# Optimization experiments

Hardware: AMD Instinct MI355X
Metric: run time of the kernel (lower is better)

## Reference

```python
import jax, jax.numpy as jnp
import numpy as np

B, TE, TD, D, U = 8, 256, 256, 256, 256


def setup_inputs() -> dict:
    key = jax.random.key(0)
    k1, k2, k3, k4, k5 = jax.random.split(key, 5)
    glorot = lambda k, shape: jax.random.uniform(
        k, shape, jnp.float32,
        -np.sqrt(6.0 / (shape[0] + shape[1])), np.sqrt(6.0 / (shape[0] + shape[1])))
    return {
        "en_seq": jax.random.normal(k1, (B, TE, D), jnp.float32),
        "de_seq": jax.random.normal(k2, (B, TD, D), jnp.float32),
        "w_en": glorot(k3, (D, U)),
        "w_de": glorot(k4, (D, U)),
        "nu": glorot(k5, (U, 1)),
    }


def reference(en_seq, de_seq, w_en, w_de, nu):
    # Additive co-attention scores.
    ae = jnp.einsum('bte,eu->btu', en_seq, w_en)          # (B, Te, U)
    ad = jnp.einsum('bsd,du->bsu', de_seq, w_de)          # (B, Td, U)
    # co_m[b, td, te, u] = ae[b, te, u] + ad[b, td, u]  (matches K.repeat / repeat_elements layout)
    co = jnp.tanh(ad[:, :, None, :] + ae[:, None, :, :])  # (B, Td, Te, U)
    mu = jnp.einsum('bstu,ul->bst', co, nu)               # (B, Td, Te)
    alphas = jax.nn.softmax(mu, axis=-1)                  # softmax over en time
    max_mu = jnp.max(mu, axis=-1)                         # (B, Td)
    max_alphas = jax.nn.softmax(max_mu, axis=-1)          # softmax over de time
    h_hat = jnp.sum(de_seq * max_alphas[..., None], axis=1)  # (B, Dd)
    sum_en = jnp.einsum('bst,bte->bse', alphas, en_seq)      # (B, Td, De)
    output = jnp.concatenate(
        [de_seq, sum_en, de_seq * sum_en, de_seq * h_hat[:, None, :]], axis=-1)
    return output  # (B, Td, 4*D)
```

## Files before the change

### kernel.cpp

```cpp
#include <hip/hip_runtime.h>

#define B_   8
#define TE_  256
#define TD_  256
#define D_   256
#define U_   256

#define EET_OFF   0
#define ED_OFF    524288
#define ALPHA_OFF 1048576
#define MAXMU_OFF 1572864
#define HH_OFF    1574912

__device__ __forceinline__ float fexp2(float x) {
#if __has_builtin(__builtin_amdgcn_exp2f)
  return __builtin_amdgcn_exp2f(x);
#else
  return exp2f(x);
#endif
}
__device__ __forceinline__ float frcp(float x) {
#if __has_builtin(__builtin_amdgcn_rcpf)
  return __builtin_amdgcn_rcpf(x);
#else
  return 1.0f / x;
#endif
}

#define LOG2E_F 1.4426950408889634f
#define TWO_LOG2E_F 2.8853900817779268f

__global__ __launch_bounds__(256) void coatt_k1_proj(
    const float* __restrict__ en, const float* __restrict__ de,
    const float* __restrict__ w_en, const float* __restrict__ w_de,
    float* __restrict__ ws) {
  const int which = blockIdx.z;
  const float* __restrict__ A = which ? de : en;
  const float* __restrict__ W = which ? w_de : w_en;
  const int rowBase = blockIdx.y * 64;
  const int colBase = blockIdx.x * 64;
  __shared__ float As[2][32][68];
  __shared__ float Bs[2][32][68];
  const int tid = threadIdx.x;
  const int tx = tid & 15, ty = tid >> 4;

  const int aRow0 = tid >> 3, aC4 = tid & 7;
  const int bK0 = tid >> 4, bC4 = tid & 15;
  float4 aR[2], bR[2];

#pragma unroll
  for (int kk = 0; kk < 2; ++kk) {
    aR[kk] = *(const float4*)&A[(rowBase + aRow0 + 32 * kk) * D_ + aC4 * 4];
    bR[kk] = *(const float4*)&W[(bK0 + 16 * kk) * U_ + colBase + bC4 * 4];
  }
#pragma unroll
  for (int kk = 0; kk < 2; ++kk) {
    float v[4]; *(float4*)v = aR[kk];
#pragma unroll
    for (int j = 0; j < 4; ++j) As[0][aC4 * 4 + j][aRow0 + 32 * kk] = v[j];
    *(float4*)&Bs[0][bK0 + 16 * kk][bC4 * 4] = bR[kk];
  }
  __syncthreads();

  float acc[4][4] = {};
#define K1_COMPUTE(BUF)                                            \
  _Pragma("unroll")                                                \
  for (int k = 0; k < 32; ++k) {                                   \
    float av[4], bv[4];                                            \
    *(float4*)av = *(const float4*)&As[BUF][k][ty * 4];            \
    *(float4*)bv = *(const float4*)&Bs[BUF][k][tx * 4];            \
    _Pragma("unroll")                                              \
    for (int i = 0; i < 4; ++i)                                    \
      _Pragma("unroll")                                            \
      for (int j = 0; j < 4; ++j)                                  \
        acc[i][j] = fmaf(av[i], bv[j], acc[i][j]);                 \
  }

  for (int kc = 0; kc < 7; ++kc) {
    const int k0 = (kc + 1) * 32;
#pragma unroll
    for (int kk = 0; kk < 2; ++kk) {
      aR[kk] = *(const float4*)&A[(rowBase + aRow0 + 32 * kk) * D_ + k0 + aC4 * 4];
      bR[kk] = *(const float4*)&W[(k0 + bK0 + 16 * kk) * U_ + colBase + bC4 * 4];
    }
    const int cur = kc & 1, nxt = cur ^ 1;
    K1_COMPUTE(cur)
#pragma unroll
    for (int kk = 0; kk < 2; ++kk) {
      float v[4]; *(float4*)v = aR[kk];
#pragma unroll
      for (int j = 0; j < 4; ++j) As[nxt][aC4 * 4 + j][aRow0 + 32 * kk] = v[j];
      *(float4*)&Bs[nxt][bK0 + 16 * kk][bC4 * 4] = bR[kk];
    }
    __syncthreads();
  }
  K1_COMPUTE(1)
  __syncthreads();

  if (which) {
    float* __restrict__ out = ws + ED_OFF;
#pragma unroll
    for (int i = 0; i < 4; ++i) {
      float4 o;
      o.x = fexp2(acc[i][0] * TWO_LOG2E_F);
      o.y = fexp2(acc[i][1] * TWO_LOG2E_F);
      o.z = fexp2(acc[i][2] * TWO_LOG2E_F);
      o.w = fexp2(acc[i][3] * TWO_LOG2E_F);
      *(float4*)&out[(rowBase + ty * 4 + i) * U_ + colBase + tx * 4] = o;
    }
  } else {
    float* Cs = &As[0][0][0];
#pragma unroll
    for (int i = 0; i < 4; ++i)
#pragma unroll
      for (int j = 0; j < 4; ++j)
        Cs[(tx * 4 + j) * 68 + ty * 4 + i] = fexp2(acc[i][j] * TWO_LOG2E_F);
    __syncthreads();
    float* __restrict__ out = ws + EET_OFF;
    const int b = rowBase >> 8, t0 = rowBase & 255;
#pragma unroll
    for (int kk = 0; kk < 4; ++kk) {
      const int q = tid + 256 * kk;
      const int uc = q >> 4, tq = q & 15;
      const float4 v = *(const float4*)&Cs[uc * 68 + tq * 4];
      *(float4*)&out[(size_t)(b * U_ + colBase + uc) * TE_ + t0 + tq * 4] = v;
    }
  }
}

__global__ __launch_bounds__(256) void coatt_k2_mu(
    const float* __restrict__ nu, float* __restrict__ ws) {
  const float* __restrict__ EeT = ws + EET_OFF;
  const float* __restrict__ Ed = ws + ED_OFF;
  float* __restrict__ alphas = ws + ALPHA_OFF;
  float* __restrict__ maxmu = ws + MAXMU_OFF;
  const int b = blockIdx.y;
  const int sBase = blockIdx.x * 4;
  const int tid = threadIdx.x;
  const int w = tid >> 6, lane = tid & 63;
  const float* __restrict__ Ee_b = EeT + (size_t)b * U_ * TE_ + tid;
  const float* __restrict__ Ed_b = Ed + (size_t)(b * TD_ + sBase) * U_;

  float acc0 = 0.f, acc1 = 0.f, acc2 = 0.f, acc3 = 0.f;
#pragma unroll 4
  for (int u4 = 0; u4 < 64; ++u4) {
    const float4 nv = *(const float4*)&nu[u4 * 4];
    const float4 e0 = *(const float4*)&Ed_b[0 * U_ + u4 * 4];
    const float4 e1 = *(const float4*)&Ed_b[1 * U_ + u4 * 4];
    const float4 e2 = *(const float4*)&Ed_b[2 * U_ + u4 * 4];
    const float4 e3 = *(const float4*)&Ed_b[3 * U_ + u4 * 4];
    float ee[4];
#pragma unroll
    for (int j = 0; j < 4; ++j) ee[j] = Ee_b[(u4 * 4 + j) * TE_];
    const float* nvp = (const float*)&nv;
    const float* p0 = (const float*)&e0;
    const float* p1 = (const float*)&e1;
    const float* p2 = (const float*)&e2;
    const float* p3 = (const float*)&e3;
#pragma unroll
    for (int j = 0; j < 4; ++j) {
      acc0 = fmaf(nvp[j], frcp(fmaf(p0[j], ee[j], 1.0f)), acc0);
      acc1 = fmaf(nvp[j], frcp(fmaf(p1[j], ee[j], 1.0f)), acc1);
      acc2 = fmaf(nvp[j], frcp(fmaf(p2[j], ee[j], 1.0f)), acc2);
      acc3 = fmaf(nvp[j], frcp(fmaf(p3[j], ee[j], 1.0f)), acc3);
    }
  }
  float v[4] = {-2.f * acc0, -2.f * acc1, -2.f * acc2, -2.f * acc3};
  __shared__ float part[4][4];
  float m[4];
#pragma unroll
  for (int s = 0; s < 4; ++s) {
    m[s] = v[s];
#pragma unroll
    for (int off = 32; off > 0; off >>= 1) m[s] = fmaxf(m[s], __shfl_xor(m[s], off));
    if (lane == 0) part[s][w] = m[s];
  }
  __syncthreads();
#pragma unroll
  for (int s = 0; s < 4; ++s)
    m[s] = fmaxf(fmaxf(part[s][0], part[s][1]), fmaxf(part[s][2], part[s][3]));
  __syncthreads();
  float e[4], sm[4];
#pragma unroll
  for (int s = 0; s < 4; ++s) {
    e[s] = fexp2((v[s] - m[s]) * LOG2E_F);
    sm[s] = e[s];
#pragma unroll
    for (int off = 32; off > 0; off >>= 1) sm[s] += __shfl_xor(sm[s], off);
    if (lane == 0) part[s][w] = sm[s];
  }
  __syncthreads();
  float* __restrict__ al = alphas + (size_t)(b * TD_ + sBase) * TE_;
#pragma unroll
  for (int s = 0; s < 4; ++s) {
    const float tot = (part[s][0] + part[s][1]) + (part[s][2] + part[s][3]);
    al[s * TE_ + tid] = e[s] * frcp(tot);
  }
  if (tid == 0) {
#pragma unroll
    for (int s = 0; s < 4; ++s) maxmu[b * TD_ + sBase + s] = m[s];
  }
}

__global__ __launch_bounds__(256) void coatt_k3_hhat(
    const float* __restrict__ de, float* __restrict__ ws) {
  const float* __restrict__ maxmu = ws + MAXMU_OFF;
  float* __restrict__ hhat = ws + HH_OFF;
  const int b = blockIdx.y;
  const int dBase = blockIdx.x * 32;
  const int tid = threadIdx.x;
  const int w = tid >> 6, lane = tid & 63;
  __shared__ float red[8];
  __shared__ float malpha[256];
  __shared__ float acc_red[256];
  const float v = maxmu[b * TD_ + tid];
  float m = v;
#pragma unroll
  for (int off = 32; off > 0; off >>= 1) m = fmaxf(m, __shfl_xor(m, off));
  if (lane == 0) red[w] = m;
  __syncthreads();
  m = fmaxf(fmaxf(red[0], red[1]), fmaxf(red[2], red[3]));
  const float e = fexp2((v - m) * LOG2E_F);
  float sm = e;
#pragma unroll
  for (int off = 32; off > 0; off >>= 1) sm += __shfl_xor(sm, off);
  if (lane == 0) red[4 + w] = sm;
  __syncthreads();
  sm = (red[4] + red[5]) + (red[6] + red[7]);
  malpha[tid] = e * frcp(sm);
  __syncthreads();
  const int dl = tid & 31, sg = tid >> 5;
  float acc = 0.f;
  for (int s = sg * 32; s < sg * 32 + 32; ++s)
    acc = fmaf(de[(b * TD_ + s) * D_ + dBase + dl], malpha[s], acc);
  acc_red[tid] = acc;
  __syncthreads();
  if (tid < 32) {
    float t = acc_red[tid];
#pragma unroll
    for (int g = 1; g < 8; ++g) t += acc_red[g * 32 + tid];
    hhat[b * D_ + dBase + tid] = t;
  }
}

__global__ __launch_bounds__(256) void coatt_k4_out(
    const float* __restrict__ en, const float* __restrict__ de,
    const float* __restrict__ ws, float* __restrict__ out) {
  const float* __restrict__ alphas = ws + ALPHA_OFF;
  const float* __restrict__ hhat = ws + HH_OFF;
  const int b = blockIdx.y;
  const int sBase = blockIdx.x * 4;
  const int d = threadIdx.x;
  const float* __restrict__ al = alphas + (size_t)(b * TD_ + sBase) * TE_;
  const float* __restrict__ en_b = en + (size_t)b * TE_ * D_ + d;

  float acc0 = 0.f, acc1 = 0.f, acc2 = 0.f, acc3 = 0.f;
#pragma unroll 4
  for (int t4 = 0; t4 < 64; ++t4) {
    const float4 a0 = *(const float4*)&al[0 * TE_ + t4 * 4];
    const float4 a1 = *(const float4*)&al[1 * TE_ + t4 * 4];
    const float4 a2 = *(const float4*)&al[2 * TE_ + t4 * 4];
    const float4 a3 = *(const float4*)&al[3 * TE_ + t4 * 4];
    float env[4];
#pragma unroll
    for (int j = 0; j < 4; ++j) env[j] = en_b[(t4 * 4 + j) * D_];
    const float* q0 = (const float*)&a0;
    const float* q1 = (const float*)&a1;
    const float* q2 = (const float*)&a2;
    const float* q3 = (const float*)&a3;
#pragma unroll
    for (int j = 0; j < 4; ++j) {
      acc0 = fmaf(q0[j], env[j], acc0);
      acc1 = fmaf(q1[j], env[j], acc1);
      acc2 = fmaf(q2[j], env[j], acc2);
      acc3 = fmaf(q3[j], env[j], acc3);
    }
  }
  const float hh = hhat[b * D_ + d];
  const float se[4] = {acc0, acc1, acc2, acc3};
#pragma unroll
  for (int s = 0; s < 4; ++s) {
    const float dd = de[(size_t)(b * TD_ + sBase + s) * D_ + d];
    float* o = out + (size_t)(b * TD_ + sBase + s) * (4 * D_);
    o[d] = dd;
    o[D_ + d] = se[s];
    o[2 * D_ + d] = dd * se[s];
    o[3 * D_ + d] = dd * hh;
  }
}

extern "C" void kernel_launch(void* const* d_in, const int* in_sizes, int n_in,
                              void* d_out, int out_size, void* d_ws, size_t ws_size,
                              hipStream_t stream) {
  (void)in_sizes; (void)n_in; (void)out_size; (void)ws_size;
  const float* en   = (const float*)d_in[0];
  const float* de   = (const float*)d_in[1];
  const float* w_en = (const float*)d_in[2];
  const float* w_de = (const float*)d_in[3];
  const float* nu   = (const float*)d_in[4];
  float* out = (float*)d_out;
  float* ws  = (float*)d_ws;

  coatt_k1_proj<<<dim3(4, 32, 2), 256, 0, stream>>>(en, de, w_en, w_de, ws);
  coatt_k2_mu<<<dim3(64, 8), 256, 0, stream>>>(nu, ws);
  coatt_k3_hhat<<<dim3(8, 8), 256, 0, stream>>>(de, ws);
  coatt_k4_out<<<dim3(64, 8), 256, 0, stream>>>(en, de, ws, out);
}
```

Before: 121.2 us.

## Fuse softmax-weighted sum into mu kernel and vectorize EeT layout

Merges the alpha softmax and the alpha-weighted sum over encoder features into one kernel, so alphas stay in shared memory instead of being written to and re-read from the workspace. The hhat kernel now writes the last output quarter directly, which removes one launch. The projection kernel moves to 512 threads with smaller per-thread tiles, and EeT is stored interleaved in groups of four u so the mu kernel can issue float4 loads. The trade-off is a longer fused kernel with more shared memory and lower per-thread GEMM reuse in the projection.

```diff
diff --git a/kernel.cpp b/kernel.cpp
--- a/kernel.cpp
+++ b/kernel.cpp
@@ -8,9 +8,7 @@
 
 #define EET_OFF   0
 #define ED_OFF    524288
-#define ALPHA_OFF 1048576
-#define MAXMU_OFF 1572864
-#define HH_OFF    1574912
+#define MAXMU_OFF 1048576
 
 __device__ __forceinline__ float fexp2(float x) {
 #if __has_builtin(__builtin_amdgcn_exp2f)
@@ -30,7 +28,7 @@
 #define LOG2E_F 1.4426950408889634f
 #define TWO_LOG2E_F 2.8853900817779268f
 
-__global__ __launch_bounds__(256) void coatt_k1_proj(
+__global__ __launch_bounds__(512) void coatt_k1_proj(
     const float* __restrict__ en, const float* __restrict__ de,
     const float* __restrict__ w_en, const float* __restrict__ w_de,
     float* __restrict__ ws) {
@@ -39,106 +37,99 @@
   const float* __restrict__ W = which ? w_de : w_en;
   const int rowBase = blockIdx.y * 64;
   const int colBase = blockIdx.x * 64;
-  __shared__ float As[2][32][68];
-  __shared__ float Bs[2][32][68];
+  __shared__ float smem[2][2][32][68];
   const int tid = threadIdx.x;
-  const int tx = tid & 15, ty = tid >> 4;
-
-  const int aRow0 = tid >> 3, aC4 = tid & 7;
-  const int bK0 = tid >> 4, bC4 = tid & 15;
-  float4 aR[2], bR[2];
-
-#pragma unroll
-  for (int kk = 0; kk < 2; ++kk) {
-    aR[kk] = *(const float4*)&A[(rowBase + aRow0 + 32 * kk) * D_ + aC4 * 4];
-    bR[kk] = *(const float4*)&W[(bK0 + 16 * kk) * U_ + colBase + bC4 * 4];
-  }
-#pragma unroll
-  for (int kk = 0; kk < 2; ++kk) {
-    float v[4]; *(float4*)v = aR[kk];
-#pragma unroll
-    for (int j = 0; j < 4; ++j) As[0][aC4 * 4 + j][aRow0 + 32 * kk] = v[j];
-    *(float4*)&Bs[0][bK0 + 16 * kk][bC4 * 4] = bR[kk];
-  }
-  __syncthreads();
-
-  float acc[4][4] = {};
-#define K1_COMPUTE(BUF)                                            \
-  _Pragma("unroll")                                                \
-  for (int k = 0; k < 32; ++k) {                                   \
-    float av[4], bv[4];                                            \
-    *(float4*)av = *(const float4*)&As[BUF][k][ty * 4];            \
-    *(float4*)bv = *(const float4*)&Bs[BUF][k][tx * 4];            \
-    _Pragma("unroll")                                              \
-    for (int i = 0; i < 4; ++i)                                    \
-      _Pragma("unroll")                                            \
-      for (int j = 0; j < 4; ++j)                                  \
-        acc[i][j] = fmaf(av[i], bv[j], acc[i][j]);                 \
+  const int tx = tid & 31, ty = tid >> 5;
+  const int aRow = tid >> 3, aC4 = tid & 7;
+  const int bK = tid >> 4, bC4 = tid & 15;
+
+  float4 aR = *(const float4*)&A[(size_t)(rowBase + aRow) * D_ + aC4 * 4];
+  float4 bR = *(const float4*)&W[(size_t)bK * U_ + colBase + bC4 * 4];
+  {
+    float v[4]; *(float4*)v = aR;
+#pragma unroll
+    for (int j = 0; j < 4; ++j) smem[0][0][aC4 * 4 + j][aRow] = v[j];
+    *(float4*)&smem[1][0][bK][bC4 * 4] = bR;
+  }
+  __syncthreads();
+
+  float acc[4][2] = {};
+#define K1_COMPUTE(BUF)                                              \
+  _Pragma("unroll")                                                  \
+  for (int k = 0; k < 32; ++k) {                                     \
+    float av[4], bv[2];                                              \
+    *(float4*)av = *(const float4*)&smem[0][BUF][k][ty * 4];         \
+    *(float2*)bv = *(const float2*)&smem[1][BUF][k][tx * 2];         \
+    _Pragma("unroll")                                                \
+    for (int i = 0; i < 4; ++i)                                      \
+      _Pragma("unroll")                                              \
+      for (int j = 0; j < 2; ++j)                                    \
+        acc[i][j] = fmaf(av[i], bv[j], acc[i][j]);                   \
   }
 
   for (int kc = 0; kc < 7; ++kc) {
     const int k0 = (kc + 1) * 32;
-#pragma unroll
-    for (int kk = 0; kk < 2; ++kk) {
-      aR[kk] = *(const float4*)&A[(rowBase + aRow0 + 32 * kk) * D_ + k0 + aC4 * 4];
-      bR[kk] = *(const float4*)&W[(k0 + bK0 + 16 * kk) * U_ + colBase + bC4 * 4];
-    }
+    aR = *(const float4*)&A[(size_t)(rowBase + aRow) * D_ + k0 + aC4 * 4];
+    bR = *(const float4*)&W[(size_t)(k0 + bK) * U_ + colBase + bC4 * 4];
     const int cur = kc & 1, nxt = cur ^ 1;
     K1_COMPUTE(cur)
-#pragma unroll
-    for (int kk = 0; kk < 2; ++kk) {
-      float v[4]; *(float4*)v = aR[kk];
-#pragma unroll
-      for (int j = 0; j < 4; ++j) As[nxt][aC4 * 4 + j][aRow0 + 32 * kk] = v[j];
-      *(float4*)&Bs[nxt][bK0 + 16 * kk][bC4 * 4] = bR[kk];
+    {
+      float v[4]; *(float4*)v = aR;
+#pragma unroll
+      for (int j = 0; j < 4; ++j) smem[0][nxt][aC4 * 4 + j][aRow] = v[j];
+      *(float4*)&smem[1][nxt][bK][bC4 * 4] = bR;
     }
     __syncthreads();
   }
   K1_COMPUTE(1)
-  __syncthreads();
 
   if (which) {
-    float* __restrict__ out = ws + ED_OFF;
+    float* __restrict__ outp = ws + ED_OFF;
 #pragma unroll
     for (int i = 0; i < 4; ++i) {
-      float4 o;
+      float2 o;
       o.x = fexp2(acc[i][0] * TWO_LOG2E_F);
       o.y = fexp2(acc[i][1] * TWO_LOG2E_F);
-      o.z = fexp2(acc[i][2] * TWO_LOG2E_F);
-      o.w = fexp2(acc[i][3] * TWO_LOG2E_F);
-      *(float4*)&out[(rowBase + ty * 4 + i) * U_ + colBase + tx * 4] = o;
+      *(float2*)&outp[(size_t)(rowBase + ty * 4 + i) * U_ + colBase + tx * 2] = o;
     }
   } else {
-    float* Cs = &As[0][0][0];
+    __syncthreads();
+    float* Cs = &smem[0][0][0][0];
 #pragma unroll
     for (int i = 0; i < 4; ++i)
 #pragma unroll
-      for (int j = 0; j < 4; ++j)
-        Cs[(tx * 4 + j) * 68 + ty * 4 + i] = fexp2(acc[i][j] * TWO_LOG2E_F);
+      for (int j = 0; j < 2; ++j)
+        Cs[(tx * 2 + j) * 69 + ty * 4 + i] = fexp2(acc[i][j] * TWO_LOG2E_F);
     __syncthreads();
-    float* __restrict__ out = ws + EET_OFF;
+    float* __restrict__ outp = ws + EET_OFF;
     const int b = rowBase >> 8, t0 = rowBase & 255;
-#pragma unroll
-    for (int kk = 0; kk < 4; ++kk) {
-      const int q = tid + 256 * kk;
-      const int uc = q >> 4, tq = q & 15;
-      const float4 v = *(const float4*)&Cs[uc * 68 + tq * 4];
-      *(float4*)&out[(size_t)(b * U_ + colBase + uc) * TE_ + t0 + tq * 4] = v;
-    }
-  }
-}
-
-__global__ __launch_bounds__(256) void coatt_k2_mu(
-    const float* __restrict__ nu, float* __restrict__ ws) {
+    const int u4Base = colBase >> 2;
+#pragma unroll
+    for (int kk = 0; kk < 2; ++kk) {
+      const int q = tid + 512 * kk;
+      const int u4l = q >> 6, tl = q & 63;
+      float4 v;
+      v.x = Cs[(u4l * 4 + 0) * 69 + tl];
+      v.y = Cs[(u4l * 4 + 1) * 69 + tl];
+      v.z = Cs[(u4l * 4 + 2) * 69 + tl];
+      v.w = Cs[(u4l * 4 + 3) * 69 + tl];
+      *(float4*)&outp[(size_t)((b * 64 + u4Base + u4l) * 256 + t0 + tl) * 4] = v;
+    }
+  }
+}
+
+__global__ __launch_bounds__(256) void coatt_k24(
+    const float* __restrict__ en, const float* __restrict__ de,
+    const float* __restrict__ nu, float* __restrict__ ws,
+    float* __restrict__ out) {
   const float* __restrict__ EeT = ws + EET_OFF;
   const float* __restrict__ Ed = ws + ED_OFF;
-  float* __restrict__ alphas = ws + ALPHA_OFF;
   float* __restrict__ maxmu = ws + MAXMU_OFF;
   const int b = blockIdx.y;
   const int sBase = blockIdx.x * 4;
   const int tid = threadIdx.x;
   const int w = tid >> 6, lane = tid & 63;
-  const float* __restrict__ Ee_b = EeT + (size_t)b * U_ * TE_ + tid;
+  const float* __restrict__ Ee_b = EeT + (size_t)b * U_ * TE_ + tid * 4;
   const float* __restrict__ Ed_b = Ed + (size_t)(b * TD_ + sBase) * U_;
 
   float acc0 = 0.f, acc1 = 0.f, acc2 = 0.f, acc3 = 0.f;
@@ -149,24 +140,24 @@
     const float4 e1 = *(const float4*)&Ed_b[1 * U_ + u4 * 4];
     const float4 e2 = *(const float4*)&Ed_b[2 * U_ + u4 * 4];
     const float4 e3 = *(const float4*)&Ed_b[3 * U_ + u4 * 4];
-    float ee[4];
-#pragma unroll
-    for (int j = 0; j < 4; ++j) ee[j] = Ee_b[(u4 * 4 + j) * TE_];
+    const float4 ee4 = *(const float4*)&Ee_b[u4 * 1024];
     const float* nvp = (const float*)&nv;
+    const float* eep = (const float*)&ee4;
     const float* p0 = (const float*)&e0;
     const float* p1 = (const float*)&e1;
     const float* p2 = (const float*)&e2;
     const float* p3 = (const float*)&e3;
 #pragma unroll
     for (int j = 0; j < 4; ++j) {
-      acc0 = fmaf(nvp[j], frcp(fmaf(p0[j], ee[j], 1.0f)), acc0);
-      acc1 = fmaf(nvp[j], frcp(fmaf(p1[j], ee[j], 1.0f)), acc1);
-      acc2 = fmaf(nvp[j], frcp(fmaf(p2[j], ee[j], 1.0f)), acc2);
-      acc3 = fmaf(nvp[j], frcp(fmaf(p3[j], ee[j], 1.0f)), acc3);
+      acc0 = fmaf(nvp[j], frcp(fmaf(p0[j], eep[j], 1.0f)), acc0);
+      acc1 = fmaf(nvp[j], frcp(fmaf(p1[j], eep[j], 1.0f)), acc1);
+      acc2 = fmaf(nvp[j], frcp(fmaf(p2[j], eep[j], 1.0f)), acc2);
+      acc3 = fmaf(nvp[j], frcp(fmaf(p3[j], eep[j], 1.0f)), acc3);
     }
   }
   float v[4] = {-2.f * acc0, -2.f * acc1, -2.f * acc2, -2.f * acc3};
   __shared__ float part[4][4];
+  __shared__ float als[4][256];
   float m[4];
 #pragma unroll
   for (int s = 0; s < 4; ++s) {
@@ -190,22 +181,56 @@
     if (lane == 0) part[s][w] = sm[s];
   }
   __syncthreads();
-  float* __restrict__ al = alphas + (size_t)(b * TD_ + sBase) * TE_;
 #pragma unroll
   for (int s = 0; s < 4; ++s) {
     const float tot = (part[s][0] + part[s][1]) + (part[s][2] + part[s][3]);
-    al[s * TE_ + tid] = e[s] * frcp(tot);
+    als[s][tid] = e[s] * frcp(tot);
   }
   if (tid == 0) {
 #pragma unroll
     for (int s = 0; s < 4; ++s) maxmu[b * TD_ + sBase + s] = m[s];
   }
+  __syncthreads();
+
+  const int d = tid;
+  const float* __restrict__ en_b = en + (size_t)b * TE_ * D_ + d;
+  float sa0 = 0.f, sa1 = 0.f, sa2 = 0.f, sa3 = 0.f;
+#pragma unroll 4
+  for (int t4 = 0; t4 < 64; ++t4) {
+    const float4 a0 = *(const float4*)&als[0][t4 * 4];
+    const float4 a1 = *(const float4*)&als[1][t4 * 4];
+    const float4 a2 = *(const float4*)&als[2][t4 * 4];
+    const float4 a3 = *(const float4*)&als[3][t4 * 4];
+    float env[4];
+#pragma unroll
+    for (int j = 0; j < 4; ++j) env[j] = en_b[(t4 * 4 + j) * D_];
+    const float* q0 = (const float*)&a0;
+    const float* q1 = (const float*)&a1;
+    const float* q2 = (const float*)&a2;
+    const float* q3 = (const float*)&a3;
+#pragma unroll
+    for (int j = 0; j < 4; ++j) {
+      sa0 = fmaf(q0[j], env[j], sa0);
+      sa1 = fmaf(q1[j], env[j], sa1);
+      sa2 = fmaf(q2[j], env[j], sa2);
+      sa3 = fmaf(q3[j], env[j], sa3);
+    }
+  }
+  const float se[4] = {sa0, sa1, sa2, sa3};
+#pragma unroll
+  for (int s = 0; s < 4; ++s) {
+    const float dd = de[(size_t)(b * TD_ + sBase + s) * D_ + d];
+    float* o = out + (size_t)(b * TD_ + sBase + s) * (4 * D_);
+    o[d] = dd;
+    o[D_ + d] = se[s];
+    o[2 * D_ + d] = dd * se[s];
+  }
 }
 
 __global__ __launch_bounds__(256) void coatt_k3_hhat(
-    const float* __restrict__ de, float* __restrict__ ws) {
+    const float* __restrict__ de, const float* __restrict__ ws,
+    float* __restrict__ out) {
   const float* __restrict__ maxmu = ws + MAXMU_OFF;
-  float* __restrict__ hhat = ws + HH_OFF;
   const int b = blockIdx.y;
   const int dBase = blockIdx.x * 32;
   const int tid = threadIdx.x;
@@ -213,14 +238,15 @@
   __shared__ float red[8];
   __shared__ float malpha[256];
   __shared__ float acc_red[256];
-  const float v = maxmu[b * TD_ + tid];
-  float m = v;
+  __shared__ float hh_s[32];
+  const float vv = maxmu[b * TD_ + tid];
+  float m = vv;
 #pragma unroll
   for (int off = 32; off > 0; off >>= 1) m = fmaxf(m, __shfl_xor(m, off));
   if (lane == 0) red[w] = m;
   __syncthreads();
   m = fmaxf(fmaxf(red[0], red[1]), fmaxf(red[2], red[3]));
-  const float e = fexp2((v - m) * LOG2E_F);
+  const float e = fexp2((vv - m) * LOG2E_F);
   float sm = e;
 #pragma unroll
   for (int off = 32; off > 0; off >>= 1) sm += __shfl_xor(sm, off);
@@ -232,60 +258,21 @@
   const int dl = tid & 31, sg = tid >> 5;
   float acc = 0.f;
   for (int s = sg * 32; s < sg * 32 + 32; ++s)
-    acc = fmaf(de[(b * TD_ + s) * D_ + dBase + dl], malpha[s], acc);
+    acc = fmaf(de[(size_t)(b * TD_ + s) * D_ + dBase + dl], malpha[s], acc);
   acc_red[tid] = acc;
   __syncthreads();
   if (tid < 32) {
     float t = acc_red[tid];
 #pragma unroll
     for (int g = 1; g < 8; ++g) t += acc_red[g * 32 + tid];
-    hhat[b * D_ + dBase + tid] = t;
-  }
-}
-
-__global__ __launch_bounds__(256) void coatt_k4_out(
-    const float* __restrict__ en, const float* __restrict__ de,
-    const float* __restrict__ ws, float* __restrict__ out) {
-  const float* __restrict__ alphas = ws + ALPHA_OFF;
-  const float* __restrict__ hhat = ws + HH_OFF;
-  const int b = blockIdx.y;
-  const int sBase = blockIdx.x * 4;
-  const int d = threadIdx.x;
-  const float* __restrict__ al = alphas + (size_t)(b * TD_ + sBase) * TE_;
-  const float* __restrict__ en_b = en + (size_t)b * TE_ * D_ + d;
-
-  float acc0 = 0.f, acc1 = 0.f, acc2 = 0.f, acc3 = 0.f;
+    hh_s[tid] = t;
+  }
+  __syncthreads();
+  const float hh = hh_s[dl];
 #pragma unroll 4
-  for (int t4 = 0; t4 < 64; ++t4) {
-    const float4 a0 = *(const float4*)&al[0 * TE_ + t4 * 4];
-    const float4 a1 = *(const float4*)&al[1 * TE_ + t4 * 4];
-    const float4 a2 = *(const float4*)&al[2 * TE_ + t4 * 4];
-    const float4 a3 = *(const float4*)&al[3 * TE_ + t4 * 4];
-    float env[4];
-#pragma unroll
-    for (int j = 0; j < 4; ++j) env[j] = en_b[(t4 * 4 + j) * D_];
-    const float* q0 = (const float*)&a0;
-    const float* q1 = (const float*)&a1;
-    const float* q2 = (const float*)&a2;
-    const float* q3 = (const float*)&a3;
-#pragma unroll
-    for (int j = 0; j < 4; ++j) {
-      acc0 = fmaf(q0[j], env[j], acc0);
-      acc1 = fmaf(q1[j], env[j], acc1);
-      acc2 = fmaf(q2[j], env[j], acc2);
-      acc3 = fmaf(q3[j], env[j], acc3);
-    }
-  }
-  const float hh = hhat[b * D_ + d];
-  const float se[4] = {acc0, acc1, acc2, acc3};
-#pragma unroll
-  for (int s = 0; s < 4; ++s) {
-    const float dd = de[(size_t)(b * TD_ + sBase + s) * D_ + d];
-    float* o = out + (size_t)(b * TD_ + sBase + s) * (4 * D_);
-    o[d] = dd;
-    o[D_ + d] = se[s];
-    o[2 * D_ + d] = dd * se[s];
-    o[3 * D_ + d] = dd * hh;
+  for (int s = sg; s < TD_; s += 8) {
+    const float dd = de[(size_t)(b * TD_ + s) * D_ + dBase + dl];
+    out[(size_t)(b * TD_ + s) * (4 * D_) + 3 * D_ + dBase + dl] = dd * hh;
   }
 }
 
@@ -301,8 +288,7 @@
   float* out = (float*)d_out;
   float* ws  = (float*)d_ws;
 
-  coatt_k1_proj<<<dim3(4, 32, 2), 256, 0, stream>>>(en, de, w_en, w_de, ws);
-  coatt_k2_mu<<<dim3(64, 8), 256, 0, stream>>>(nu, ws);
-  coatt_k3_hhat<<<dim3(8, 8), 256, 0, stream>>>(de, ws);
-  coatt_k4_out<<<dim3(64, 8), 256, 0, stream>>>(en, de, ws, out);
-}
+  coatt_k1_proj<<<dim3(4, 32, 2), 512, 0, stream>>>(en, de, w_en, w_de, ws);
+  coatt_k24<<<dim3(64, 8), 256, 0, stream>>>(en, de, nu, ws, out);
+  coatt_k3_hhat<<<dim3(8, 8), 256, 0, stream>>>(de, ws, out);
+}
```

New measurement: 114.4 us. 5.6% less time.
